# Optimization experiments

Hardware: AMD Instinct MI355X
Metric: run time of the kernel (lower is better)

The kernel has to match this reference:

```python
import jax, jax.numpy as jnp
import numpy as np

V, E, H, N, L = 32000, 512, 512, 64, 128


def setup_inputs() -> dict:
    key = jax.random.key(0)
    ks = jax.random.split(key, 16)
    s = 0.02  # init scale
    return {
        "input_ids": jax.random.randint(ks[0], (N,), 0, V),
        "h": jax.random.normal(ks[1], (N, H), jnp.float32),
        "c": jax.random.normal(ks[2], (N, H), jnp.float32),
        "encoder_hiddens": jax.random.normal(ks[3], (N, L, H), jnp.float32),
        "attn_mask": jnp.zeros((N, L), dtype=bool),
        "embed_W": jax.random.normal(ks[4], (V, E), jnp.float32) * s,
        "w_ih": jax.random.normal(ks[5], (4 * H, E), jnp.float32) * s,
        "b_ih": jnp.zeros((4 * H,), jnp.float32),
        "w_hh": jax.random.normal(ks[6], (4 * H, H), jnp.float32) * s,
        "b_hh": jnp.zeros((4 * H,), jnp.float32),
        "attn_Wh": jax.random.normal(ks[7], (H, H), jnp.float32) * s,
        "attn_Ws": jax.random.normal(ks[8], (H, H), jnp.float32) * s,
        "attn_v": jax.random.normal(ks[9], (H,), jnp.float32) * s,
        "h2o_W": jax.random.normal(ks[10], (V, 2 * H), jnp.float32) * s,
        "h2o_b": jnp.zeros((V,), jnp.float32),
    }


def reference(input_ids, h, c, encoder_hiddens, attn_mask, embed_W,
              w_ih, b_ih, w_hh, b_hh, attn_Wh, attn_Ws, attn_v,
              h2o_W, h2o_b):
    # Embedding lookup: (N, E)
    emb = embed_W[input_ids]
    # LSTM cell: fused gate GEMMs, chunk order i, f, g, o (torch chunk(4))
    gates = emb @ w_ih.T + b_ih + h @ w_hh.T + b_hh  # (N, 4H)
    i_g, f_g, g_g, o_g = jnp.split(gates, 4, axis=1)
    c_t = jax.nn.sigmoid(f_g) * c + jax.nn.sigmoid(i_g) * jnp.tanh(g_g)
    h_t = jax.nn.sigmoid(o_g) * jnp.tanh(c_t)  # (N, H)
    # Bahdanau attention: v^T tanh(W_h h_t + W_s enc)
    proj = jnp.tanh((h_t @ attn_Wh.T)[:, None, :] + encoder_hiddens @ attn_Ws.T)  # (N, L, H)
    score = jnp.einsum('nlh,h->nl', proj, attn_v)  # (N, L)
    score = jnp.where(attn_mask, -jnp.inf, score)
    attn_w = jax.nn.softmax(score, axis=1)  # (N, L)
    context = jnp.einsum('nl,nlh->nh', attn_w, encoder_hiddens)  # (N, H)
    # Output projection + log-softmax over vocab
    combined = jnp.concatenate([h_t, context], axis=1)  # (N, 2H)
    out = jax.nn.log_softmax(combined @ h2o_W.T + h2o_b, axis=-1)  # (N, V)
    return out, h_t, c_t
```

## Files before the change

### kernel.cpp

```cpp
#include <hip/hip_runtime.h>
#include <math.h>

#define V 32000
#define E 512
#define H 512
#define N 64
#define L 128
#define NV (N*V)
#define NH (N*H)
#define MTOT (N*L)
#define VT 500

typedef short  s8v  __attribute__((ext_vector_type(8)));
typedef float  f4v  __attribute__((ext_vector_type(4)));

__device__ __forceinline__ float sigf(float x) { return 1.0f / (1.0f + __expf(-x)); }

__device__ __forceinline__ unsigned short f2bf(float f) {
    unsigned int u = __float_as_uint(f);
    unsigned int r = u + 0x7FFFu + ((u >> 16) & 1u);
    return (unsigned short)(r >> 16);
}

__global__ __launch_bounds__(256) void k_gates(
    const int* __restrict__ ids, const float* __restrict__ hprev,
    const float* __restrict__ embW, const float* __restrict__ w_ih,
    const float* __restrict__ w_hh, float* __restrict__ gates_p)
{
    __shared__ __align__(16) float xs[64 * 128];
    const int bx = blockIdx.x;
    const int ks = blockIdx.y;
    const int tid = threadIdx.x;
    const bool emb_part = (ks < 4);
    const int koff = (ks & 3) * 128;

    for (int i = tid; i < 64 * 32; i += 256) {
        int n = i >> 5, kk4 = i & 31;
        float4 x4;
        if (emb_part)
            x4 = ((const float4*)(embW + (size_t)ids[n] * E + koff))[kk4];
        else
            x4 = ((const float4*)(hprev + (size_t)n * H + koff))[kk4];
        ((float4*)xs)[n * 32 + kk4] = x4;
    }
    __syncthreads();

    const int jl = tid & 63;
    const int ng = tid >> 6;
    const int j = bx * 64 + jl;
    const int nb = ng * 16;
    const float* wrow = (emb_part ? w_ih : w_hh) + (size_t)j * 512 + koff;

    float acc[16];
#pragma unroll
    for (int i = 0; i < 16; ++i) acc[i] = 0.f;

    for (int e4 = 0; e4 < 32; ++e4) {
        float4 w4 = ((const float4*)wrow)[e4];
#pragma unroll
        for (int i = 0; i < 16; ++i) {
            float4 x4 = ((const float4*)xs)[(nb + i) * 32 + e4];
            acc[i] += w4.x * x4.x + w4.y * x4.y + w4.z * x4.z + w4.w * x4.w;
        }
    }
#pragma unroll
    for (int i = 0; i < 16; ++i)
        gates_p[(size_t)ks * (64 * 2048) + (size_t)(nb + i) * 2048 + j] = acc[i];
}

__global__ __launch_bounds__(256) void k_lstm_pw(
    const float* __restrict__ gates_p, const float* __restrict__ b_ih,
    const float* __restrict__ b_hh, const float* __restrict__ cprev,
    float* __restrict__ out, unsigned short* __restrict__ xb)
{
    int i = blockIdx.x * 256 + threadIdx.x;
    if (i >= NH) return;
    int n = i >> 9, k = i & 511;
    float g[4];
#pragma unroll
    for (int q = 0; q < 4; ++q) {
        int j = q * 512 + k;
        float s = b_ih[j] + b_hh[j];
#pragma unroll
        for (int ks = 0; ks < 8; ++ks)
            s += gates_p[(size_t)ks * (64 * 2048) + (size_t)n * 2048 + j];
        g[q] = s;
    }
    float ig = sigf(g[0]), fg = sigf(g[1]), gg = tanhf(g[2]), og = sigf(g[3]);
    float ct = fg * cprev[i] + ig * gg;
    float ht = og * tanhf(ct);
    out[NV + i] = ht;
    out[NV + NH + i] = ct;
    xb[(size_t)n * 1024 + k] = f2bf(ht);
}

__global__ __launch_bounds__(256) void k_sproj(
    const float* __restrict__ out, const float* __restrict__ Wh,
    float* __restrict__ sproj)
{
    __shared__ __align__(16) float xs[512];
    int n = blockIdx.x >> 1;
    int h = (blockIdx.x & 1) * 256 + threadIdx.x;
    const float* ht = out + NV + (size_t)n * 512;
    for (int i = threadIdx.x; i < 512; i += 256) xs[i] = ht[i];
    __syncthreads();
    const float* wrow = Wh + (size_t)h * 512;
    float acc = 0.f;
    for (int e4 = 0; e4 < 128; ++e4) {
        float4 w4 = ((const float4*)wrow)[e4];
        float4 x4 = ((const float4*)xs)[e4];
        acc += w4.x * x4.x + w4.y * x4.y + w4.z * x4.z + w4.w * x4.w;
    }
    sproj[(size_t)n * 512 + h] = acc;
}

__global__ __launch_bounds__(256) void k_score_gemm(
    const float* __restrict__ enc, const float* __restrict__ Ws,
    const float* __restrict__ sproj, const float* __restrict__ av,
    float* __restrict__ scorep)
{
    __shared__ __align__(16) short As[64 * 72];
    __shared__ __align__(16) short Bs[64 * 72];
    __shared__ float sred[64];

    const int bm = blockIdx.x, bh = blockIdx.y;
    const int tid = threadIdx.x;
    const int w = tid >> 6, l = tid & 63;
    const int wave_m = (w >> 1) * 32, wave_h = (w & 1) * 32;
    const int lq = l >> 4, lr = l & 15;

    if (tid < 64) sred[tid] = 0.f;

    f4v acc[2][2];
#pragma unroll
    for (int i = 0; i < 2; ++i)
#pragma unroll
        for (int j = 0; j < 2; ++j) acc[i][j] = (f4v)0.f;

    for (int kt = 0; kt < 8; ++kt) {
        __syncthreads();
#pragma unroll
        for (int r = 0; r < 2; ++r) {
            int idx = (r * 256 + tid) * 8;
            int row = idx >> 6, col = idx & 63;
            const float* sa = enc + (size_t)(bm * 64 + row) * 512 + kt * 64 + col;
            const float* sb = Ws  + (size_t)(bh * 64 + row) * 512 + kt * 64 + col;
            float4 a0 = *(const float4*)sa, a1 = *(const float4*)(sa + 4);
            float4 b0 = *(const float4*)sb, b1 = *(const float4*)(sb + 4);
            union { unsigned short u[8]; uint4 q; } pa, pb;
            pa.u[0]=f2bf(a0.x); pa.u[1]=f2bf(a0.y); pa.u[2]=f2bf(a0.z); pa.u[3]=f2bf(a0.w);
            pa.u[4]=f2bf(a1.x); pa.u[5]=f2bf(a1.y); pa.u[6]=f2bf(a1.z); pa.u[7]=f2bf(a1.w);
            pb.u[0]=f2bf(b0.x); pb.u[1]=f2bf(b0.y); pb.u[2]=f2bf(b0.z); pb.u[3]=f2bf(b0.w);
            pb.u[4]=f2bf(b1.x); pb.u[5]=f2bf(b1.y); pb.u[6]=f2bf(b1.z); pb.u[7]=f2bf(b1.w);
            *(uint4*)(As + row * 72 + col) = pa.q;
            *(uint4*)(Bs + row * 72 + col) = pb.q;
        }
        __syncthreads();

#pragma unroll
        for (int ks = 0; ks < 2; ++ks) {
            s8v a_frag[2], b_frag[2];
#pragma unroll
            for (int i = 0; i < 2; ++i)
                a_frag[i] = *(const s8v*)(As + (wave_m + 16 * i + lr) * 72 + ks * 32 + lq * 8);
#pragma unroll
            for (int j = 0; j < 2; ++j)
                b_frag[j] = *(const s8v*)(Bs + (wave_h + 16 * j + lr) * 72 + ks * 32 + lq * 8);
#pragma unroll
            for (int i = 0; i < 2; ++i)
#pragma unroll
                for (int j = 0; j < 2; ++j)
                    acc[i][j] = __builtin_amdgcn_mfma_f32_16x16x32_bf16(
                        a_frag[i], b_frag[j], acc[i][j], 0, 0, 0);
        }
    }
    __syncthreads();

    const int hc0 = bh * 64 + wave_h + lr;
#pragma unroll
    for (int i = 0; i < 2; ++i) {
#pragma unroll
        for (int reg = 0; reg < 4; ++reg) {
            int m_local = wave_m + 16 * i + lq * 4 + reg;
            int m = bm * 64 + m_local;
            int n = m >> 7;
            float p = 0.f;
#pragma unroll
            for (int j = 0; j < 2; ++j) {
                int hc = hc0 + 16 * j;
                float val = acc[i][j][reg] + sproj[(size_t)n * 512 + hc];
                p += tanhf(val) * av[hc];
            }
            p += __shfl_xor(p, 1, 64);
            p += __shfl_xor(p, 2, 64);
            p += __shfl_xor(p, 4, 64);
            p += __shfl_xor(p, 8, 64);
            if (lr == 0) atomicAdd(&sred[m_local], p);
        }
    }
    __syncthreads();
    if (tid < 64)
        scorep[(size_t)bh * MTOT + bm * 64 + tid] = sred[tid];
}

__global__ __launch_bounds__(512) void k_softmax_ctx(
    const float* __restrict__ scorep, const unsigned char* __restrict__ mask,
    const float* __restrict__ enc, unsigned short* __restrict__ xb)
{
    __shared__ float sc[128];
    __shared__ float wl[128];
    const int n = blockIdx.x, t = threadIdx.x;

    if (t < 128) {
        float s = 0.f;
#pragma unroll
        for (int q = 0; q < 8; ++q)
            s += scorep[(size_t)q * MTOT + n * 128 + t];
        if (mask[(size_t)n * 128 + t]) s = -1e30f;
        sc[t] = s;
    }
    __syncthreads();
    if (t < 64) {
        float m = fmaxf(sc[t], sc[t + 64]);
#pragma unroll
        for (int off = 32; off > 0; off >>= 1) m = fmaxf(m, __shfl_xor(m, off, 64));
        float e0 = __expf(sc[t] - m), e1 = __expf(sc[t + 64] - m);
        float ss = e0 + e1;
#pragma unroll
        for (int off = 32; off > 0; off >>= 1) ss += __shfl_xor(ss, off, 64);
        float inv = 1.0f / ss;
        wl[t] = e0 * inv;
        wl[t + 64] = e1 * inv;
    }
    __syncthreads();

    const float* encn = enc + (size_t)n * L * H + t;
    float acc = 0.f;
#pragma unroll 4
    for (int ll = 0; ll < 128; ++ll)
        acc += wl[ll] * encn[(size_t)ll * 512];
    xb[(size_t)n * 1024 + 512 + t] = f2bf(acc);
}

__global__ __launch_bounds__(256) void k_logits(
    const float* __restrict__ h2oW, const unsigned short* __restrict__ xb,
    const float* __restrict__ h2ob, float* __restrict__ dlogits,
    float* __restrict__ pmax, float* __restrict__ psum)
{
    __shared__ __align__(16) short As[64 * 72];
    __shared__ __align__(16) short Bs[64 * 72];
    __shared__ __align__(16) float cs[64 * 68];

    const int bm = blockIdx.x;
    const int tid = threadIdx.x;
    const int w = tid >> 6, l = tid & 63;
    const int wave_m = (w & 1) * 32, wave_n = (w >> 1) * 32;
    const int lq = l >> 4, lr = l & 15;

    const int arow = tid >> 2;
    const int acol = (tid & 3) * 16;
    const float* aptr = h2oW + (size_t)(bm * 64 + arow) * 1024 + acol;
    const unsigned short* bptr = xb + (size_t)arow * 1024 + acol;

    f4v acc[2][2];
#pragma unroll
    for (int i = 0; i < 2; ++i)
#pragma unroll
        for (int j = 0; j < 2; ++j) acc[i][j] = (f4v)0.f;

    float4 ra[4];
    uint4  rb[2];
#pragma unroll
    for (int r = 0; r < 4; ++r) ra[r] = ((const float4*)aptr)[r];
    rb[0] = *(const uint4*)bptr;
    rb[1] = *(const uint4*)(bptr + 8);

#pragma unroll 1
    for (int kt = 0; kt < 16; ++kt) {
        if (kt) __syncthreads();
        union { unsigned short u[8]; uint4 q; } p0, p1;
        p0.u[0]=f2bf(ra[0].x); p0.u[1]=f2bf(ra[0].y); p0.u[2]=f2bf(ra[0].z); p0.u[3]=f2bf(ra[0].w);
        p0.u[4]=f2bf(ra[1].x); p0.u[5]=f2bf(ra[1].y); p0.u[6]=f2bf(ra[1].z); p0.u[7]=f2bf(ra[1].w);
        p1.u[0]=f2bf(ra[2].x); p1.u[1]=f2bf(ra[2].y); p1.u[2]=f2bf(ra[2].z); p1.u[3]=f2bf(ra[2].w);
        p1.u[4]=f2bf(ra[3].x); p1.u[5]=f2bf(ra[3].y); p1.u[6]=f2bf(ra[3].z); p1.u[7]=f2bf(ra[3].w);
        *(uint4*)(As + arow * 72 + acol)     = p0.q;
        *(uint4*)(As + arow * 72 + acol + 8) = p1.q;
        *(uint4*)(Bs + arow * 72 + acol)     = rb[0];
        *(uint4*)(Bs + arow * 72 + acol + 8) = rb[1];
        __syncthreads();

        if (kt < 15) {
            const float* ap = aptr + (kt + 1) * 64;
            const unsigned short* bp = bptr + (kt + 1) * 64;
#pragma unroll
            for (int r = 0; r < 4; ++r) ra[r] = ((const float4*)ap)[r];
            rb[0] = *(const uint4*)bp;
            rb[1] = *(const uint4*)(bp + 8);
        }

#pragma unroll
        for (int ks = 0; ks < 2; ++ks) {
            s8v a_frag[2], b_frag[2];
#pragma unroll
            for (int i = 0; i < 2; ++i)
                a_frag[i] = *(const s8v*)(As + (wave_m + 16 * i + lr) * 72 + ks * 32 + lq * 8);
#pragma unroll
            for (int j = 0; j < 2; ++j)
                b_frag[j] = *(const s8v*)(Bs + (wave_n + 16 * j + lr) * 72 + ks * 32 + lq * 8);
#pragma unroll
            for (int i = 0; i < 2; ++i)
#pragma unroll
                for (int j = 0; j < 2; ++j)
                    acc[i][j] = __builtin_amdgcn_mfma_f32_16x16x32_bf16(
                        a_frag[i], b_frag[j], acc[i][j], 0, 0, 0);
        }
    }
    __syncthreads();

#pragma unroll
    for (int i = 0; i < 2; ++i)
#pragma unroll
        for (int j = 0; j < 2; ++j)
#pragma unroll
            for (int reg = 0; reg < 4; ++reg)
                cs[(wave_n + 16 * j + lr) * 68 + wave_m + 16 * i + lq * 4 + reg] = acc[i][j][reg];
    __syncthreads();

    const int n = tid >> 2, q = tid & 3;
    const int v0 = bm * 64 + q * 16;
    float4 vals[4];
    float m_loc = -1e30f;
#pragma unroll
    for (int k = 0; k < 4; ++k) {
        float4 cv = *(const float4*)(cs + n * 68 + q * 16 + 4 * k);
        float4 bv = *(const float4*)(h2ob + v0 + 4 * k);
        cv.x += bv.x; cv.y += bv.y; cv.z += bv.z; cv.w += bv.w;
        vals[k] = cv;
        *(float4*)(dlogits + (size_t)n * V + v0 + 4 * k) = cv;
        m_loc = fmaxf(m_loc, fmaxf(fmaxf(cv.x, cv.y), fmaxf(cv.z, cv.w)));
    }
    float s_loc = 0.f;
#pragma unroll
    for (int k = 0; k < 4; ++k) {
        s_loc += __expf(vals[k].x - m_loc) + __expf(vals[k].y - m_loc)
               + __expf(vals[k].z - m_loc) + __expf(vals[k].w - m_loc);
    }
    float m2 = fmaxf(m_loc, __shfl_xor(m_loc, 1, 64));
    m2 = fmaxf(m2, __shfl_xor(m2, 2, 64));
    s_loc *= __expf(m_loc - m2);
    float s2 = s_loc + __shfl_xor(s_loc, 1, 64);
    s2 += __shfl_xor(s2, 2, 64);
    if (q == 0) {
        pmax[(size_t)n * VT + bm] = m2;
        psum[(size_t)n * VT + bm] = s2;
    }
}

__global__ __launch_bounds__(256) void k_lse(
    const float* __restrict__ pmax, const float* __restrict__ psum,
    float* __restrict__ lse)
{
    __shared__ float rm[4], rs[4];
    const int n = blockIdx.x, t = threadIdx.x;
    float m0 = (t < VT) ? pmax[(size_t)n * VT + t] : -1e30f;
    float m1 = (t + 256 < VT) ? pmax[(size_t)n * VT + t + 256] : -1e30f;
    float mm = fmaxf(m0, m1);
#pragma unroll
    for (int off = 32; off > 0; off >>= 1) mm = fmaxf(mm, __shfl_xor(mm, off, 64));
    if ((t & 63) == 0) rm[t >> 6] = mm;
    __syncthreads();
    float m = fmaxf(fmaxf(rm[0], rm[1]), fmaxf(rm[2], rm[3]));

    float s = 0.f;
    if (t < VT)       s += psum[(size_t)n * VT + t] * __expf(m0 - m);
    if (t + 256 < VT) s += psum[(size_t)n * VT + t + 256] * __expf(m1 - m);
#pragma unroll
    for (int off = 32; off > 0; off >>= 1) s += __shfl_xor(s, off, 64);
    if ((t & 63) == 0) rs[t >> 6] = s;
    __syncthreads();
    if (t == 0) {
        float st = rs[0] + rs[1] + rs[2] + rs[3];
        lse[n] = m + __logf(st);
    }
}

__global__ __launch_bounds__(256) void k_norm(
    float* __restrict__ dlogits, const float* __restrict__ lse)
{
    const int n = blockIdx.y;
    const int t4 = blockIdx.x * 256 + threadIdx.x;
    if (t4 >= V / 4) return;
    float s = lse[n];
    float4* p = (float4*)(dlogits + (size_t)n * V) + t4;
    float4 v = *p;
    v.x -= s; v.y -= s; v.z -= s; v.w -= s;
    *p = v;
}

extern "C" void kernel_launch(void* const* d_in, const int* in_sizes, int n_in,
                              void* d_out, int out_size, void* d_ws, size_t ws_size,
                              hipStream_t stream)
{
    const int* ids   = (const int*)d_in[0];
    const float* h   = (const float*)d_in[1];
    const float* c   = (const float*)d_in[2];
    const float* enc = (const float*)d_in[3];
    const unsigned char* mask = (const unsigned char*)d_in[4];
    const float* embW = (const float*)d_in[5];
    const float* w_ih = (const float*)d_in[6];
    const float* b_ih = (const float*)d_in[7];
    const float* w_hh = (const float*)d_in[8];
    const float* b_hh = (const float*)d_in[9];
    const float* Wh   = (const float*)d_in[10];
    const float* Ws   = (const float*)d_in[11];
    const float* av   = (const float*)d_in[12];
    const float* h2oW = (const float*)d_in[13];
    const float* h2ob = (const float*)d_in[14];

    float* out = (float*)d_out;
    float* ws = (float*)d_ws;
    float* gates_p = ws;
    float* sproj   = ws + 1048576;
    float* scorep  = ws + 1048576 + 32768;
    unsigned short* xb = (unsigned short*)(ws + 1048576 + 32768 + 65536);
    float* pmax = ws;
    float* psum = ws + 32000;
    float* lse  = ws + 64000;

    k_gates<<<dim3(32, 8), 256, 0, stream>>>(ids, h, embW, w_ih, w_hh, gates_p);
    k_lstm_pw<<<128, 256, 0, stream>>>(gates_p, b_ih, b_hh, c, out, xb);
    k_sproj<<<128, 256, 0, stream>>>(out, Wh, sproj);
    k_score_gemm<<<dim3(128, 8), 256, 0, stream>>>(enc, Ws, sproj, av, scorep);
    k_softmax_ctx<<<64, 512, 0, stream>>>(scorep, mask, enc, xb);
    k_logits<<<VT, 256, 0, stream>>>(h2oW, xb, h2ob, out, pmax, psum);
    k_lse<<<64, 256, 0, stream>>>(pmax, psum, lse);
    k_norm<<<dim3(32, 64), 256, 0, stream>>>(out, lse);
}
```

Measured before the change: 348.5 us.

## Pre-convert encoder and Ws to bf16, prefetch score tiles, halve logits tile

A new prep kernel converts encoder_hiddens and attn_Ws to bf16 once per call. The score GEMM then loads bf16 tiles with register prefetch of the next k-tile, and the context reduction reads bf16 encoder values. Each tile was previously re-converted from fp32 by every block that used it, so this cuts redundant global fp32 reads and conversion work, at the cost of an extra kernel pass and workspace writes. Separately, the logits kernel switches to 32-row vocab tiles with 128 threads and 1000 blocks to get more parallelism, which means more partial max/sum entries for the LSE kernel to reduce.

```diff
diff --git a/kernel.cpp b/kernel.cpp
--- a/kernel.cpp
+++ b/kernel.cpp
@@ -9,7 +9,7 @@
 #define NV (N*V)
 #define NH (N*H)
 #define MTOT (N*L)
-#define VT 500
+#define VT 1000
 
 typedef short  s8v  __attribute__((ext_vector_type(8)));
 typedef float  f4v  __attribute__((ext_vector_type(4)));
@@ -20,6 +20,27 @@
     unsigned int u = __float_as_uint(f);
     unsigned int r = u + 0x7FFFu + ((u >> 16) & 1u);
     return (unsigned short)(r >> 16);
+}
+__device__ __forceinline__ float bf2f(unsigned short u) {
+    return __uint_as_float(((unsigned int)u) << 16);
+}
+
+__global__ __launch_bounds__(256) void k_prep(
+    const float* __restrict__ enc, const float* __restrict__ Ws,
+    unsigned short* __restrict__ encb, unsigned short* __restrict__ Wsb)
+{
+    size_t g = (size_t)blockIdx.x * 256 + threadIdx.x;
+    const float* src;
+    unsigned short* dst;
+    size_t off;
+    if (g < (size_t)N * L * H / 8) { src = enc; dst = encb; off = g * 8; }
+    else { src = Ws; dst = Wsb; off = (g - (size_t)N * L * H / 8) * 8; }
+    float4 a = ((const float4*)(src + off))[0];
+    float4 b = ((const float4*)(src + off))[1];
+    union { unsigned short u[8]; uint4 q; } p;
+    p.u[0]=f2bf(a.x); p.u[1]=f2bf(a.y); p.u[2]=f2bf(a.z); p.u[3]=f2bf(a.w);
+    p.u[4]=f2bf(b.x); p.u[5]=f2bf(b.y); p.u[6]=f2bf(b.z); p.u[7]=f2bf(b.w);
+    *(uint4*)(dst + off) = p.q;
 }
 
 __global__ __launch_bounds__(256) void k_gates(
@@ -115,7 +136,7 @@
 }
 
 __global__ __launch_bounds__(256) void k_score_gemm(
-    const float* __restrict__ enc, const float* __restrict__ Ws,
+    const unsigned short* __restrict__ encb, const unsigned short* __restrict__ Wsb,
     const float* __restrict__ sproj, const float* __restrict__ av,
     float* __restrict__ scorep)
 {
@@ -129,6 +150,11 @@
     const int wave_m = (w >> 1) * 32, wave_h = (w & 1) * 32;
     const int lq = l >> 4, lr = l & 15;
 
+    const int arow = tid >> 2;
+    const int acol = (tid & 3) * 16;
+    const unsigned short* aptr = encb + (size_t)(bm * 64 + arow) * 512 + acol;
+    const unsigned short* bptr = Wsb  + (size_t)(bh * 64 + arow) * 512 + acol;
+
     if (tid < 64) sred[tid] = 0.f;
 
     f4v acc[2][2];
@@ -137,25 +163,25 @@
 #pragma unroll
         for (int j = 0; j < 2; ++j) acc[i][j] = (f4v)0.f;
 
+    uint4 ra[2], rb[2];
+    ra[0] = ((const uint4*)aptr)[0]; ra[1] = ((const uint4*)aptr)[1];
+    rb[0] = ((const uint4*)bptr)[0]; rb[1] = ((const uint4*)bptr)[1];
+
+#pragma unroll 1
     for (int kt = 0; kt < 8; ++kt) {
+        if (kt) __syncthreads();
+        *(uint4*)(As + arow * 72 + acol)     = ra[0];
+        *(uint4*)(As + arow * 72 + acol + 8) = ra[1];
+        *(uint4*)(Bs + arow * 72 + acol)     = rb[0];
+        *(uint4*)(Bs + arow * 72 + acol + 8) = rb[1];
         __syncthreads();
-#pragma unroll
-        for (int r = 0; r < 2; ++r) {
-            int idx = (r * 256 + tid) * 8;
-            int row = idx >> 6, col = idx & 63;
-            const float* sa = enc + (size_t)(bm * 64 + row) * 512 + kt * 64 + col;
-            const float* sb = Ws  + (size_t)(bh * 64 + row) * 512 + kt * 64 + col;
-            float4 a0 = *(const float4*)sa, a1 = *(const float4*)(sa + 4);
-            float4 b0 = *(const float4*)sb, b1 = *(const float4*)(sb + 4);
-            union { unsigned short u[8]; uint4 q; } pa, pb;
-            pa.u[0]=f2bf(a0.x); pa.u[1]=f2bf(a0.y); pa.u[2]=f2bf(a0.z); pa.u[3]=f2bf(a0.w);
-            pa.u[4]=f2bf(a1.x); pa.u[5]=f2bf(a1.y); pa.u[6]=f2bf(a1.z); pa.u[7]=f2bf(a1.w);
-            pb.u[0]=f2bf(b0.x); pb.u[1]=f2bf(b0.y); pb.u[2]=f2bf(b0.z); pb.u[3]=f2bf(b0.w);
-            pb.u[4]=f2bf(b1.x); pb.u[5]=f2bf(b1.y); pb.u[6]=f2bf(b1.z); pb.u[7]=f2bf(b1.w);
-            *(uint4*)(As + row * 72 + col) = pa.q;
-            *(uint4*)(Bs + row * 72 + col) = pb.q;
-        }
-        __syncthreads();
+
+        if (kt < 7) {
+            const unsigned short* ap = aptr + (kt + 1) * 64;
+            const unsigned short* bp = bptr + (kt + 1) * 64;
+            ra[0] = ((const uint4*)ap)[0]; ra[1] = ((const uint4*)ap)[1];
+            rb[0] = ((const uint4*)bp)[0]; rb[1] = ((const uint4*)bp)[1];
+        }
 
 #pragma unroll
         for (int ks = 0; ks < 2; ++ks) {
@@ -205,7 +231,7 @@
 
 __global__ __launch_bounds__(512) void k_softmax_ctx(
     const float* __restrict__ scorep, const unsigned char* __restrict__ mask,
-    const float* __restrict__ enc, unsigned short* __restrict__ xb)
+    const unsigned short* __restrict__ encb, unsigned short* __restrict__ xb)
 {
     __shared__ float sc[128];
     __shared__ float wl[128];
@@ -234,33 +260,36 @@
     }
     __syncthreads();
 
-    const float* encn = enc + (size_t)n * L * H + t;
+    const unsigned short* encn = encb + (size_t)n * L * H + t;
     float acc = 0.f;
 #pragma unroll 4
     for (int ll = 0; ll < 128; ++ll)
-        acc += wl[ll] * encn[(size_t)ll * 512];
+        acc += wl[ll] * bf2f(encn[(size_t)ll * 512]);
     xb[(size_t)n * 1024 + 512 + t] = f2bf(acc);
 }
 
-__global__ __launch_bounds__(256) void k_logits(
+__global__ __launch_bounds__(128) void k_logits(
     const float* __restrict__ h2oW, const unsigned short* __restrict__ xb,
     const float* __restrict__ h2ob, float* __restrict__ dlogits,
     float* __restrict__ pmax, float* __restrict__ psum)
 {
-    __shared__ __align__(16) short As[64 * 72];
-    __shared__ __align__(16) short Bs[64 * 72];
-    __shared__ __align__(16) float cs[64 * 68];
+    __shared__ __align__(16) char smem[32 * 72 * 2 + 64 * 72 * 2];
+    short* As = (short*)smem;
+    short* Bs = (short*)(smem + 32 * 72 * 2);
+    float* cs = (float*)smem;
 
     const int bm = blockIdx.x;
     const int tid = threadIdx.x;
     const int w = tid >> 6, l = tid & 63;
-    const int wave_m = (w & 1) * 32, wave_n = (w >> 1) * 32;
+    const int wave_n = w * 32;
     const int lq = l >> 4, lr = l & 15;
 
     const int arow = tid >> 2;
     const int acol = (tid & 3) * 16;
-    const float* aptr = h2oW + (size_t)(bm * 64 + arow) * 1024 + acol;
-    const unsigned short* bptr = xb + (size_t)arow * 1024 + acol;
+    const int brow = tid >> 1;
+    const int bcol = (tid & 1) * 32;
+    const float* aptr = h2oW + (size_t)(bm * 32 + arow) * 1024 + acol;
+    const unsigned short* bptr = xb + (size_t)brow * 1024 + bcol;
 
     f4v acc[2][2];
 #pragma unroll
@@ -269,11 +298,11 @@
         for (int j = 0; j < 2; ++j) acc[i][j] = (f4v)0.f;
 
     float4 ra[4];
-    uint4  rb[2];
+    uint4  rb[4];
 #pragma unroll
     for (int r = 0; r < 4; ++r) ra[r] = ((const float4*)aptr)[r];
-    rb[0] = *(const uint4*)bptr;
-    rb[1] = *(const uint4*)(bptr + 8);
+#pragma unroll
+    for (int r = 0; r < 4; ++r) rb[r] = ((const uint4*)bptr)[r];
 
 #pragma unroll 1
     for (int kt = 0; kt < 16; ++kt) {
@@ -285,8 +314,9 @@
         p1.u[4]=f2bf(ra[3].x); p1.u[5]=f2bf(ra[3].y); p1.u[6]=f2bf(ra[3].z); p1.u[7]=f2bf(ra[3].w);
         *(uint4*)(As + arow * 72 + acol)     = p0.q;
         *(uint4*)(As + arow * 72 + acol + 8) = p1.q;
-        *(uint4*)(Bs + arow * 72 + acol)     = rb[0];
-        *(uint4*)(Bs + arow * 72 + acol + 8) = rb[1];
+#pragma unroll
+        for (int r = 0; r < 4; ++r)
+            *(uint4*)(Bs + brow * 72 + bcol + 8 * r) = rb[r];
         __syncthreads();
 
         if (kt < 15) {
@@ -294,8 +324,8 @@
             const unsigned short* bp = bptr + (kt + 1) * 64;
 #pragma unroll
             for (int r = 0; r < 4; ++r) ra[r] = ((const float4*)ap)[r];
-            rb[0] = *(const uint4*)bp;
-            rb[1] = *(const uint4*)(bp + 8);
+#pragma unroll
+            for (int r = 0; r < 4; ++r) rb[r] = ((const uint4*)bp)[r];
         }
 
 #pragma unroll
@@ -303,7 +333,7 @@
             s8v a_frag[2], b_frag[2];
 #pragma unroll
             for (int i = 0; i < 2; ++i)
-                a_frag[i] = *(const s8v*)(As + (wave_m + 16 * i + lr) * 72 + ks * 32 + lq * 8);
+                a_frag[i] = *(const s8v*)(As + (16 * i + lr) * 72 + ks * 32 + lq * 8);
 #pragma unroll
             for (int j = 0; j < 2; ++j)
                 b_frag[j] = *(const s8v*)(Bs + (wave_n + 16 * j + lr) * 72 + ks * 32 + lq * 8);
@@ -323,16 +353,16 @@
         for (int j = 0; j < 2; ++j)
 #pragma unroll
             for (int reg = 0; reg < 4; ++reg)
-                cs[(wave_n + 16 * j + lr) * 68 + wave_m + 16 * i + lq * 4 + reg] = acc[i][j][reg];
-    __syncthreads();
-
-    const int n = tid >> 2, q = tid & 3;
-    const int v0 = bm * 64 + q * 16;
+                cs[(wave_n + 16 * j + lr) * 36 + 16 * i + lq * 4 + reg] = acc[i][j][reg];
+    __syncthreads();
+
+    const int n = tid >> 1, q = tid & 1;
+    const int v0 = bm * 32 + q * 16;
     float4 vals[4];
     float m_loc = -1e30f;
 #pragma unroll
     for (int k = 0; k < 4; ++k) {
-        float4 cv = *(const float4*)(cs + n * 68 + q * 16 + 4 * k);
+        float4 cv = *(const float4*)(cs + n * 36 + q * 16 + 4 * k);
         float4 bv = *(const float4*)(h2ob + v0 + 4 * k);
         cv.x += bv.x; cv.y += bv.y; cv.z += bv.z; cv.w += bv.w;
         vals[k] = cv;
@@ -346,10 +376,8 @@
                + __expf(vals[k].z - m_loc) + __expf(vals[k].w - m_loc);
     }
     float m2 = fmaxf(m_loc, __shfl_xor(m_loc, 1, 64));
-    m2 = fmaxf(m2, __shfl_xor(m2, 2, 64));
     s_loc *= __expf(m_loc - m2);
     float s2 = s_loc + __shfl_xor(s_loc, 1, 64);
-    s2 += __shfl_xor(s2, 2, 64);
     if (q == 0) {
         pmax[(size_t)n * VT + bm] = m2;
         psum[(size_t)n * VT + bm] = s2;
@@ -362,9 +390,14 @@
 {
     __shared__ float rm[4], rs[4];
     const int n = blockIdx.x, t = threadIdx.x;
-    float m0 = (t < VT) ? pmax[(size_t)n * VT + t] : -1e30f;
-    float m1 = (t + 256 < VT) ? pmax[(size_t)n * VT + t + 256] : -1e30f;
-    float mm = fmaxf(m0, m1);
+    float pm[4], ps[4];
+#pragma unroll
+    for (int k = 0; k < 4; ++k) {
+        int idx = t + 256 * k;
+        pm[k] = (idx < VT) ? pmax[(size_t)n * VT + idx] : -1e30f;
+        ps[k] = (idx < VT) ? psum[(size_t)n * VT + idx] : 0.f;
+    }
+    float mm = fmaxf(fmaxf(pm[0], pm[1]), fmaxf(pm[2], pm[3]));
 #pragma unroll
     for (int off = 32; off > 0; off >>= 1) mm = fmaxf(mm, __shfl_xor(mm, off, 64));
     if ((t & 63) == 0) rm[t >> 6] = mm;
@@ -372,8 +405,8 @@
     float m = fmaxf(fmaxf(rm[0], rm[1]), fmaxf(rm[2], rm[3]));
 
     float s = 0.f;
-    if (t < VT)       s += psum[(size_t)n * VT + t] * __expf(m0 - m);
-    if (t + 256 < VT) s += psum[(size_t)n * VT + t + 256] * __expf(m1 - m);
+#pragma unroll
+    for (int k = 0; k < 4; ++k) s += ps[k] * __expf(pm[k] - m);
 #pragma unroll
     for (int off = 32; off > 0; off >>= 1) s += __shfl_xor(s, off, 64);
     if ((t & 63) == 0) rs[t >> 6] = s;
@@ -422,17 +455,20 @@
     float* gates_p = ws;
     float* sproj   = ws + 1048576;
     float* scorep  = ws + 1048576 + 32768;
-    unsigned short* xb = (unsigned short*)(ws + 1048576 + 32768 + 65536);
+    unsigned short* xb   = (unsigned short*)(ws + 1146880);
+    unsigned short* encb = (unsigned short*)(ws + 1179648);
+    unsigned short* Wsb  = (unsigned short*)(ws + 3276800);
     float* pmax = ws;
-    float* psum = ws + 32000;
-    float* lse  = ws + 64000;
-
+    float* psum = ws + 64000;
+    float* lse  = ws + 128000;
+
+    k_prep<<<2176, 256, 0, stream>>>(enc, Ws, encb, Wsb);
     k_gates<<<dim3(32, 8), 256, 0, stream>>>(ids, h, embW, w_ih, w_hh, gates_p);
     k_lstm_pw<<<128, 256, 0, stream>>>(gates_p, b_ih, b_hh, c, out, xb);
     k_sproj<<<128, 256, 0, stream>>>(out, Wh, sproj);
-    k_score_gemm<<<dim3(128, 8), 256, 0, stream>>>(enc, Ws, sproj, av, scorep);
-    k_softmax_ctx<<<64, 512, 0, stream>>>(scorep, mask, enc, xb);
-    k_logits<<<VT, 256, 0, stream>>>(h2oW, xb, h2ob, out, pmax, psum);
+    k_score_gemm<<<dim3(128, 8), 256, 0, stream>>>(encb, Wsb, sproj, av, scorep);
+    k_softmax_ctx<<<64, 512, 0, stream>>>(scorep, mask, encb, xb);
+    k_logits<<<VT, 128, 0, stream>>>(h2oW, xb, h2ob, out, pmax, psum);
     k_lse<<<64, 256, 0, stream>>>(pmax, psum, lse);
     k_norm<<<dim3(32, 64), 256, 0, stream>>>(out, lse);
 }
```

After: 387.8 us. 1.11x slower.
